# Performance work log

Hardware: AMD Instinct MI355X
Metric: run time of the kernel (lower is better)

## Reference

```python
import jax, jax.numpy as jnp
import numpy as np

WIN = 64
DF = 512
NH = 8
DH = DF // NH


def setup_inputs() -> dict:
    key = jax.random.key(0)
    k1, k2, k3, k4, k5 = jax.random.split(key, 5)
    b, n_p = 8, 4096
    x = jax.random.normal(k1, (b, n_p, DF), dtype=jnp.float32)
    z = jax.random.normal(k2, (b, n_p, DF), dtype=jnp.float32)
    # torch nn.Linear weights: [out_features, in_features]
    w_qkv = jax.random.normal(k3, (3 * DF, DF), dtype=jnp.float32) * (DF ** -0.5)
    proj_w = jax.random.normal(k4, (DF, DF), dtype=jnp.float32) * (DF ** -0.5)
    proj_b = jax.random.normal(k5, (DF,), dtype=jnp.float32) * 0.01
    return {"x": x, "z": z, "w_qkv": w_qkv, "proj_w": proj_w, "proj_b": proj_b}


def reference(x, z, w_qkv, proj_w, proj_b):
    b, n_p, _ = x.shape
    n_w, w_s = n_p // WIN, WIN
    scale = DH ** -0.5
    # QKV projection (no bias): [b, n_p, 3*DF]
    qkv = jnp.einsum('bnd,ed->bne', x, w_qkv)
    qkv = qkv.reshape(b, n_w, w_s, 3, NH, DH)
    q = qkv[:, :, :, 0]  # [b, n_w, w_s, NH, DH]
    k = qkv[:, :, :, 1]
    v = qkv[:, :, :, 2]
    # per-window attention scores: [b, n_w, NH, w_s, w_s]
    attn = scale * jnp.einsum('bwqhd,bwkhd->bwhqk', q, k)
    attn = jax.nn.softmax(attn, axis=-1)
    out = jnp.einsum('bwhqk,bwkhd->bwqhd', attn, v)  # [b, n_w, w_s, NH, DH]
    out = out.reshape(b, n_p, DF)
    out = jnp.einsum('bnd,ed->bne', out, proj_w) + proj_b
    return out
```

## Files before the change

### kernel.cpp

```cpp
#include <hip/hip_runtime.h>
#include <hip/hip_bf16.h>
#include <stdint.h>

#define NP 4096
#define DF 512
#define NQ3 1536

using bf16x8 = __attribute__((ext_vector_type(8))) short;
using f32x4  = __attribute__((ext_vector_type(4))) float;

static __device__ __forceinline__ f32x4 mfma16(bf16x8 a, bf16x8 b, f32x4 c) {
    return __builtin_amdgcn_mfma_f32_16x16x32_bf16(a, b, c, 0, 0, 0);
}
static __device__ __forceinline__ f32x4 zero4() { f32x4 z = {0.f,0.f,0.f,0.f}; return z; }

static __device__ __forceinline__ int SWZ64(int row, int col) {
    return (row * 64 + col) ^ ((row & 7) << 3);
}

static __device__ __forceinline__ unsigned short f2bf(float f) {
    __hip_bfloat16 h = __float2bfloat16(f);
    return reinterpret_cast<unsigned short&>(h);
}

#define GLOAD_LDS16(gp, lp) __builtin_amdgcn_global_load_lds( \
    (const __attribute__((address_space(1))) uint32_t*)(gp), \
    (__attribute__((address_space(3))) uint32_t*)(lp), 16, 0, 0)

__global__ void convert_all(const float* __restrict__ x,
                            const float* __restrict__ wqkv,
                            const float* __restrict__ projw,
                            unsigned short* __restrict__ xb,
                            unsigned short* __restrict__ wqb,
                            unsigned short* __restrict__ pwb) {
    const int XQ = (8 * NP * DF) / 4;
    const int WQ = (3 * DF * DF) / 4;
    const int PQ = (DF * DF) / 4;
    int i = blockIdx.x * blockDim.x + threadIdx.x;
    const float* src; unsigned short* dst; int j;
    if (i < XQ)                { src = x;     dst = xb;  j = i; }
    else if (i < XQ + WQ)      { src = wqkv;  dst = wqb; j = i - XQ; }
    else if (i < XQ + WQ + PQ) { src = projw; dst = pwb; j = i - XQ - WQ; }
    else return;
    float4 v = *(const float4*)(src + (size_t)j * 4);
    ushort4 o;
    o.x = f2bf(v.x); o.y = f2bf(v.y); o.z = f2bf(v.z); o.w = f2bf(v.w);
    *(ushort4*)(dst + (size_t)j * 4) = o;
}

__launch_bounds__(256, 2)
__global__ void qkv_gemm(const __hip_bfloat16* __restrict__ A,
                         const __hip_bfloat16* __restrict__ Bt,
                         unsigned short* __restrict__ C) {
    __shared__ __hip_bfloat16 As[128 * 64];
    __shared__ __hip_bfloat16 Bs[128 * 64];

    const int tid  = threadIdx.x;
    const int wid  = tid >> 6;
    const int lane = tid & 63;
    const int ln16 = lane & 15;
    const int lg   = lane >> 4;
    const int wr   = wid >> 1;
    const int wc   = wid & 1;

    int wk = (blockIdx.x & 7) * 384 + (blockIdx.x >> 3);
    const int m0 = (wk / 12) * 128;
    const int n0 = (wk % 12) * 128;

    f32x4 acc[4][4];
    #pragma unroll
    for (int i = 0; i < 4; ++i)
        #pragma unroll
        for (int j = 0; j < 4; ++j) acc[i][j] = zero4();

    for (int kt = 0; kt < 8; ++kt) {
        int k0 = kt * 64;
        #pragma unroll
        for (int it = 0; it < 4; ++it) {
            int slot = it * 256 + tid;
            int row  = slot >> 3;
            int c    = slot & 7;
            int gc   = (c ^ (row & 7)) * 8;
            GLOAD_LDS16(A  + (size_t)(m0 + row) * DF + k0 + gc, &As[slot * 8]);
            GLOAD_LDS16(Bt + (size_t)(n0 + row) * DF + k0 + gc, &Bs[slot * 8]);
        }
        __syncthreads();
        #pragma unroll
        for (int kk = 0; kk < 2; ++kk) {
            int c0 = kk * 4 + lg;
            bf16x8 af[4], bfr[4];
            #pragma unroll
            for (int rt = 0; rt < 4; ++rt) {
                int r = wr * 64 + rt * 16 + ln16;
                af[rt] = *(const bf16x8*)&As[(r << 6) + ((c0 ^ (r & 7)) << 3)];
            }
            #pragma unroll
            for (int ct = 0; ct < 4; ++ct) {
                int r = wc * 64 + ct * 16 + ln16;
                bfr[ct] = *(const bf16x8*)&Bs[(r << 6) + ((c0 ^ (r & 7)) << 3)];
            }
            #pragma unroll
            for (int rt = 0; rt < 4; ++rt)
                #pragma unroll
                for (int ct = 0; ct < 4; ++ct)
                    acc[rt][ct] = mfma16(af[rt], bfr[ct], acc[rt][ct]);
        }
        __syncthreads();
    }

    #pragma unroll
    for (int rt = 0; rt < 4; ++rt)
        #pragma unroll
        for (int ct = 0; ct < 4; ++ct)
            #pragma unroll
            for (int j = 0; j < 4; ++j)
                C[(size_t)(m0 + wr * 64 + rt * 16 + lg * 4 + j) * NQ3
                  + n0 + wc * 64 + ct * 16 + ln16] = f2bf(acc[rt][ct][j]);
}

__launch_bounds__(256, 2)
__global__ void attn(const __hip_bfloat16* __restrict__ qkv,
                     unsigned short* __restrict__ aout) {
    __shared__ unsigned short lds[4][2][64 * 64];

    const int tid  = threadIdx.x;
    const int wid  = tid >> 6;
    const int lane = tid & 63;
    const int ln16 = lane & 15;
    const int lg   = lane >> 4;

    const int blk = blockIdx.x;
    const int bw  = blk >> 1;
    const int hh  = (blk & 1) * 4 + wid;
    const size_t tokbase = (size_t)bw * 64;
    const __hip_bfloat16* base = qkv + tokbase * NQ3;

    #pragma unroll
    for (int rt = 0; rt < 4; ++rt)
        #pragma unroll
        for (int ks = 0; ks < 2; ++ks) {
            bf16x8 vf = *(const bf16x8*)(base + (size_t)(rt * 16 + ln16) * NQ3
                                         + 2 * DF + hh * 64 + ks * 32 + lg * 8);
            #pragma unroll
            for (int i = 0; i < 8; ++i) {
                int d = ks * 32 + lg * 8 + i;
                lds[wid][1][SWZ64(d, rt * 16 + ln16)] = (unsigned short)vf[i];
            }
        }

    bf16x8 kf[4][2];
    #pragma unroll
    for (int ct = 0; ct < 4; ++ct)
        #pragma unroll
        for (int ks = 0; ks < 2; ++ks)
            kf[ct][ks] = *(const bf16x8*)(base + (size_t)(ct * 16 + ln16) * NQ3
                                          + DF + hh * 64 + ks * 32 + lg * 8);

    const float scale = 0.125f;
    #pragma unroll
    for (int rt = 0; rt < 4; ++rt) {
        bf16x8 qf[2];
        #pragma unroll
        for (int ks = 0; ks < 2; ++ks)
            qf[ks] = *(const bf16x8*)(base + (size_t)(rt * 16 + ln16) * NQ3
                                      + hh * 64 + ks * 32 + lg * 8);
        f32x4 s[4];
        #pragma unroll
        for (int ct = 0; ct < 4; ++ct) s[ct] = zero4();
        #pragma unroll
        for (int ks = 0; ks < 2; ++ks)
            #pragma unroll
            for (int ct = 0; ct < 4; ++ct)
                s[ct] = mfma16(qf[ks], kf[ct][ks], s[ct]);
        #pragma unroll
        for (int j = 0; j < 4; ++j) {
            float sv[4];
            float m = -1e30f;
            #pragma unroll
            for (int ct = 0; ct < 4; ++ct) { sv[ct] = s[ct][j] * scale; m = fmaxf(m, sv[ct]); }
            #pragma unroll
            for (int off = 1; off < 16; off <<= 1) m = fmaxf(m, __shfl_xor(m, off));
            float pv[4], sum = 0.f;
            #pragma unroll
            for (int ct = 0; ct < 4; ++ct) { pv[ct] = __expf(sv[ct] - m); sum += pv[ct]; }
            #pragma unroll
            for (int off = 1; off < 16; off <<= 1) sum += __shfl_xor(sum, off);
            float inv = 1.f / sum;
            int q = rt * 16 + lg * 4 + j;
            #pragma unroll
            for (int ct = 0; ct < 4; ++ct)
                lds[wid][0][SWZ64(q, ct * 16 + ln16)] = f2bf(pv[ct] * inv);
        }
    }

    bf16x8 vtf[4][2];
    #pragma unroll
    for (int ct = 0; ct < 4; ++ct)
        #pragma unroll
        for (int ks = 0; ks < 2; ++ks)
            vtf[ct][ks] = *(const bf16x8*)&lds[wid][1][SWZ64(ct * 16 + ln16,
                                                             ks * 32 + lg * 8)];
    #pragma unroll
    for (int rt = 0; rt < 4; ++rt) {
        bf16x8 pf[2];
        #pragma unroll
        for (int ks = 0; ks < 2; ++ks)
            pf[ks] = *(const bf16x8*)&lds[wid][0][SWZ64(rt * 16 + ln16,
                                                        ks * 32 + lg * 8)];
        f32x4 o[4];
        #pragma unroll
        for (int ct = 0; ct < 4; ++ct) o[ct] = zero4();
        #pragma unroll
        for (int ks = 0; ks < 2; ++ks)
            #pragma unroll
            for (int ct = 0; ct < 4; ++ct)
                o[ct] = mfma16(pf[ks], vtf[ct][ks], o[ct]);
        #pragma unroll
        for (int ct = 0; ct < 4; ++ct)
            #pragma unroll
            for (int j = 0; j < 4; ++j)
                aout[(tokbase + rt * 16 + lg * 4 + j) * DF + hh * 64
                     + ct * 16 + ln16] = f2bf(o[ct][j]);
    }
}

__launch_bounds__(256, 4)
__global__ void proj_gemm(const __hip_bfloat16* __restrict__ A,
                          const __hip_bfloat16* __restrict__ Bt,
                          const float* __restrict__ bias,
                          float* __restrict__ out) {
    __shared__ __hip_bfloat16 As[128 * 64];
    __shared__ __hip_bfloat16 Bs[128 * 64];

    const int tid  = threadIdx.x;
    const int wid  = tid >> 6;
    const int lane = tid & 63;
    const int ln16 = lane & 15;
    const int lg   = lane >> 4;
    const int wr   = wid >> 1;
    const int wc   = wid & 1;

    int wk = (blockIdx.x & 7) * 128 + (blockIdx.x >> 3);
    const int m0  = (wk >> 2) * 128;
    const int n0g = (wk & 3) * 128;

    f32x4 acc[4][4];
    #pragma unroll
    for (int i = 0; i < 4; ++i)
        #pragma unroll
        for (int j = 0; j < 4; ++j) acc[i][j] = zero4();

    for (int kt = 0; kt < 8; ++kt) {
        int k0 = kt * 64;
        #pragma unroll
        for (int it = 0; it < 4; ++it) {
            int slot = it * 256 + tid;
            int row  = slot >> 3;
            int c    = slot & 7;
            int gc   = (c ^ (row & 7)) * 8;
            GLOAD_LDS16(A  + (size_t)(m0  + row) * DF + k0 + gc, &As[slot * 8]);
            GLOAD_LDS16(Bt + (size_t)(n0g + row) * DF + k0 + gc, &Bs[slot * 8]);
        }
        __syncthreads();
        #pragma unroll
        for (int kk = 0; kk < 2; ++kk) {
            int c0 = kk * 4 + lg;
            bf16x8 af[4], bfr[4];
            #pragma unroll
            for (int rt = 0; rt < 4; ++rt) {
                int r = wr * 64 + rt * 16 + ln16;
                af[rt] = *(const bf16x8*)&As[(r << 6) + ((c0 ^ (r & 7)) << 3)];
            }
            #pragma unroll
            for (int ct = 0; ct < 4; ++ct) {
                int r = wc * 64 + ct * 16 + ln16;
                bfr[ct] = *(const bf16x8*)&Bs[(r << 6) + ((c0 ^ (r & 7)) << 3)];
            }
            #pragma unroll
            for (int rt = 0; rt < 4; ++rt)
                #pragma unroll
                for (int ct = 0; ct < 4; ++ct)
                    acc[rt][ct] = mfma16(af[rt], bfr[ct], acc[rt][ct]);
        }
        __syncthreads();
    }

    #pragma unroll
    for (int ct = 0; ct < 4; ++ct) {
        int col = n0g + wc * 64 + ct * 16 + ln16;
        float bv = bias[col];
        #pragma unroll
        for (int rt = 0; rt < 4; ++rt)
            #pragma unroll
            for (int j = 0; j < 4; ++j)
                out[(size_t)(m0 + wr * 64 + rt * 16 + lg * 4 + j) * DF + col] =
                    acc[rt][ct][j] + bv;
    }
}

extern "C" void kernel_launch(void* const* d_in, const int* in_sizes, int n_in,
                              void* d_out, int out_size, void* d_ws, size_t ws_size,
                              hipStream_t stream) {
    const float* x      = (const float*)d_in[0];
    const float* w_qkv  = (const float*)d_in[2];
    const float* proj_w = (const float*)d_in[3];
    const float* proj_b = (const float*)d_in[4];
    float* outp = (float*)d_out;

    const size_t NTOK = (size_t)8 * NP;
    unsigned short* xb   = (unsigned short*)d_ws;
    unsigned short* qkvb = xb + NTOK * DF;
    unsigned short* wqb  = qkvb + NTOK * NQ3;
    unsigned short* pwb  = wqb + 3 * DF * DF;
    unsigned short* aout = xb;

    convert_all<<<8704, 512, 0, stream>>>(x, w_qkv, proj_w, xb, wqb, pwb);

    qkv_gemm<<<3072, 256, 0, stream>>>((const __hip_bfloat16*)xb,
                                       (const __hip_bfloat16*)wqb, qkvb);

    attn<<<1024, 256, 0, stream>>>((const __hip_bfloat16*)qkvb, aout);

    proj_gemm<<<1024, 256, 0, stream>>>((const __hip_bfloat16*)aout,
                                        (const __hip_bfloat16*)pwb,
                                        proj_b, outp);
}
```

Baseline: 131.1 us.

## Fuse x conversion into QKV GEMM and projection into attention kernel

Drops the separate fp32-to-bf16 pass over x: the QKV GEMM now loads fp32 x directly, converts it in registers and writes swizzled bf16 into LDS. The attention kernel now handles all 8 heads of a window per 512-thread block, stages each head's output in LDS, and runs the output projection plus bias in-block, so the standalone projection GEMM and its intermediate global round trip go away. In exchange, x is reread as fp32 once per column tile of the QKV GEMM instead of as bf16, that A tile no longer uses the async global-to-LDS path, and the projection reads weights straight from global memory without LDS reuse.

```diff
diff --git a/kernel.cpp b/kernel.cpp
--- a/kernel.cpp
+++ b/kernel.cpp
@@ -7,6 +7,7 @@
 #define NQ3 1536
 
 using bf16x8 = __attribute__((ext_vector_type(8))) short;
+using u16x8  = __attribute__((ext_vector_type(8))) unsigned short;
 using f32x4  = __attribute__((ext_vector_type(4))) float;
 
 static __device__ __forceinline__ f32x4 mfma16(bf16x8 a, bf16x8 b, f32x4 c) {
@@ -27,20 +28,16 @@
     (const __attribute__((address_space(1))) uint32_t*)(gp), \
     (__attribute__((address_space(3))) uint32_t*)(lp), 16, 0, 0)
 
-__global__ void convert_all(const float* __restrict__ x,
-                            const float* __restrict__ wqkv,
-                            const float* __restrict__ projw,
-                            unsigned short* __restrict__ xb,
-                            unsigned short* __restrict__ wqb,
-                            unsigned short* __restrict__ pwb) {
-    const int XQ = (8 * NP * DF) / 4;
+__global__ void convert_weights(const float* __restrict__ wqkv,
+                                const float* __restrict__ projw,
+                                unsigned short* __restrict__ wqb,
+                                unsigned short* __restrict__ pwb) {
     const int WQ = (3 * DF * DF) / 4;
     const int PQ = (DF * DF) / 4;
     int i = blockIdx.x * blockDim.x + threadIdx.x;
     const float* src; unsigned short* dst; int j;
-    if (i < XQ)                { src = x;     dst = xb;  j = i; }
-    else if (i < XQ + WQ)      { src = wqkv;  dst = wqb; j = i - XQ; }
-    else if (i < XQ + WQ + PQ) { src = projw; dst = pwb; j = i - XQ - WQ; }
+    if (i < WQ)           { src = wqkv;  dst = wqb; j = i; }
+    else if (i < WQ + PQ) { src = projw; dst = pwb; j = i - WQ; }
     else return;
     float4 v = *(const float4*)(src + (size_t)j * 4);
     ushort4 o;
@@ -49,7 +46,7 @@
 }
 
 __launch_bounds__(256, 2)
-__global__ void qkv_gemm(const __hip_bfloat16* __restrict__ A,
+__global__ void qkv_gemm(const float* __restrict__ A,
                          const __hip_bfloat16* __restrict__ Bt,
                          unsigned short* __restrict__ C) {
     __shared__ __hip_bfloat16 As[128 * 64];
@@ -81,8 +78,20 @@
             int row  = slot >> 3;
             int c    = slot & 7;
             int gc   = (c ^ (row & 7)) * 8;
-            GLOAD_LDS16(A  + (size_t)(m0 + row) * DF + k0 + gc, &As[slot * 8]);
             GLOAD_LDS16(Bt + (size_t)(n0 + row) * DF + k0 + gc, &Bs[slot * 8]);
+        }
+        #pragma unroll
+        for (int it = 0; it < 4; ++it) {
+            int slot = it * 256 + tid;
+            int row  = slot >> 3;
+            int c    = slot & 7;
+            const float* gp = A + (size_t)(m0 + row) * DF + k0 + c * 8;
+            float4 v0 = *(const float4*)gp;
+            float4 v1 = *(const float4*)(gp + 4);
+            u16x8 u;
+            u[0] = f2bf(v0.x); u[1] = f2bf(v0.y); u[2] = f2bf(v0.z); u[3] = f2bf(v0.w);
+            u[4] = f2bf(v1.x); u[5] = f2bf(v1.y); u[6] = f2bf(v1.z); u[7] = f2bf(v1.w);
+            *(u16x8*)&As[row * 64 + (c ^ (row & 7)) * 8] = u;
         }
         __syncthreads();
         #pragma unroll
@@ -118,10 +127,12 @@
                   + n0 + wc * 64 + ct * 16 + ln16] = f2bf(acc[rt][ct][j]);
 }
 
-__launch_bounds__(256, 2)
-__global__ void attn(const __hip_bfloat16* __restrict__ qkv,
-                     unsigned short* __restrict__ aout) {
-    __shared__ unsigned short lds[4][2][64 * 64];
+__launch_bounds__(512, 2)
+__global__ void attn_proj(const __hip_bfloat16* __restrict__ qkv,
+                          const __hip_bfloat16* __restrict__ pw,
+                          const float* __restrict__ bias,
+                          float* __restrict__ out) {
+    __shared__ unsigned short lds[8][2][64 * 64];
 
     const int tid  = threadIdx.x;
     const int wid  = tid >> 6;
@@ -129,11 +140,10 @@
     const int ln16 = lane & 15;
     const int lg   = lane >> 4;
 
-    const int blk = blockIdx.x;
-    const int bw  = blk >> 1;
-    const int hh  = (blk & 1) * 4 + wid;
+    const int bw = blockIdx.x;
     const size_t tokbase = (size_t)bw * 64;
     const __hip_bfloat16* base = qkv + tokbase * NQ3;
+    const int hh = wid;
 
     #pragma unroll
     for (int rt = 0; rt < 4; ++rt)
@@ -144,7 +154,7 @@
             #pragma unroll
             for (int i = 0; i < 8; ++i) {
                 int d = ks * 32 + lg * 8 + i;
-                lds[wid][1][SWZ64(d, rt * 16 + ln16)] = (unsigned short)vf[i];
+                lds[hh][1][SWZ64(d, rt * 16 + ln16)] = (unsigned short)vf[i];
             }
         }
 
@@ -189,7 +199,7 @@
             int q = rt * 16 + lg * 4 + j;
             #pragma unroll
             for (int ct = 0; ct < 4; ++ct)
-                lds[wid][0][SWZ64(q, ct * 16 + ln16)] = f2bf(pv[ct] * inv);
+                lds[hh][0][SWZ64(q, ct * 16 + ln16)] = f2bf(pv[ct] * inv);
         }
     }
 
@@ -198,15 +208,15 @@
     for (int ct = 0; ct < 4; ++ct)
         #pragma unroll
         for (int ks = 0; ks < 2; ++ks)
-            vtf[ct][ks] = *(const bf16x8*)&lds[wid][1][SWZ64(ct * 16 + ln16,
-                                                             ks * 32 + lg * 8)];
+            vtf[ct][ks] = *(const bf16x8*)&lds[hh][1][SWZ64(ct * 16 + ln16,
+                                                            ks * 32 + lg * 8)];
     #pragma unroll
     for (int rt = 0; rt < 4; ++rt) {
         bf16x8 pf[2];
         #pragma unroll
         for (int ks = 0; ks < 2; ++ks)
-            pf[ks] = *(const bf16x8*)&lds[wid][0][SWZ64(rt * 16 + ln16,
-                                                        ks * 32 + lg * 8)];
+            pf[ks] = *(const bf16x8*)&lds[hh][0][SWZ64(rt * 16 + ln16,
+                                                       ks * 32 + lg * 8)];
         f32x4 o[4];
         #pragma unroll
         for (int ct = 0; ct < 4; ++ct) o[ct] = zero4();
@@ -219,82 +229,48 @@
         for (int ct = 0; ct < 4; ++ct)
             #pragma unroll
             for (int j = 0; j < 4; ++j)
-                aout[(tokbase + rt * 16 + lg * 4 + j) * DF + hh * 64
-                     + ct * 16 + ln16] = f2bf(o[ct][j]);
-    }
-}
-
-__launch_bounds__(256, 4)
-__global__ void proj_gemm(const __hip_bfloat16* __restrict__ A,
-                          const __hip_bfloat16* __restrict__ Bt,
-                          const float* __restrict__ bias,
-                          float* __restrict__ out) {
-    __shared__ __hip_bfloat16 As[128 * 64];
-    __shared__ __hip_bfloat16 Bs[128 * 64];
-
-    const int tid  = threadIdx.x;
-    const int wid  = tid >> 6;
-    const int lane = tid & 63;
-    const int ln16 = lane & 15;
-    const int lg   = lane >> 4;
-    const int wr   = wid >> 1;
-    const int wc   = wid & 1;
-
-    int wk = (blockIdx.x & 7) * 128 + (blockIdx.x >> 3);
-    const int m0  = (wk >> 2) * 128;
-    const int n0g = (wk & 3) * 128;
-
-    f32x4 acc[4][4];
+                lds[hh][1][SWZ64(rt * 16 + lg * 4 + j, ct * 16 + ln16)] =
+                    f2bf(o[ct][j]);
+    }
+    __syncthreads();
+
+    f32x4 oacc[4][4];
     #pragma unroll
     for (int i = 0; i < 4; ++i)
         #pragma unroll
-        for (int j = 0; j < 4; ++j) acc[i][j] = zero4();
-
-    for (int kt = 0; kt < 8; ++kt) {
-        int k0 = kt * 64;
-        #pragma unroll
-        for (int it = 0; it < 4; ++it) {
-            int slot = it * 256 + tid;
-            int row  = slot >> 3;
-            int c    = slot & 7;
-            int gc   = (c ^ (row & 7)) * 8;
-            GLOAD_LDS16(A  + (size_t)(m0  + row) * DF + k0 + gc, &As[slot * 8]);
-            GLOAD_LDS16(Bt + (size_t)(n0g + row) * DF + k0 + gc, &Bs[slot * 8]);
-        }
-        __syncthreads();
+        for (int j = 0; j < 4; ++j) oacc[i][j] = zero4();
+
+    for (int h2 = 0; h2 < 8; ++h2) {
         #pragma unroll
         for (int kk = 0; kk < 2; ++kk) {
-            int c0 = kk * 4 + lg;
-            bf16x8 af[4], bfr[4];
-            #pragma unroll
-            for (int rt = 0; rt < 4; ++rt) {
-                int r = wr * 64 + rt * 16 + ln16;
-                af[rt] = *(const bf16x8*)&As[(r << 6) + ((c0 ^ (r & 7)) << 3)];
-            }
+            int kl = kk * 32 + lg * 8;
+            bf16x8 a[4];
+            #pragma unroll
+            for (int rt = 0; rt < 4; ++rt)
+                a[rt] = *(const bf16x8*)&lds[h2][1][SWZ64(rt * 16 + ln16, kl)];
             #pragma unroll
             for (int ct = 0; ct < 4; ++ct) {
-                int r = wc * 64 + ct * 16 + ln16;
-                bfr[ct] = *(const bf16x8*)&Bs[(r << 6) + ((c0 ^ (r & 7)) << 3)];
-            }
-            #pragma unroll
-            for (int rt = 0; rt < 4; ++rt)
+                const __hip_bfloat16* prow =
+                    (const __hip_bfloat16*)pw
+                    + ((size_t)(wid * 64 + ct * 16 + ln16)) * DF + h2 * 64 + kl;
+                bf16x8 bfr = *(const bf16x8*)prow;
                 #pragma unroll
-                for (int ct = 0; ct < 4; ++ct)
-                    acc[rt][ct] = mfma16(af[rt], bfr[ct], acc[rt][ct]);
-        }
-        __syncthreads();
+                for (int rt = 0; rt < 4; ++rt)
+                    oacc[rt][ct] = mfma16(a[rt], bfr, oacc[rt][ct]);
+            }
+        }
     }
 
     #pragma unroll
     for (int ct = 0; ct < 4; ++ct) {
-        int col = n0g + wc * 64 + ct * 16 + ln16;
+        int col = wid * 64 + ct * 16 + ln16;
         float bv = bias[col];
         #pragma unroll
         for (int rt = 0; rt < 4; ++rt)
             #pragma unroll
             for (int j = 0; j < 4; ++j)
-                out[(size_t)(m0 + wr * 64 + rt * 16 + lg * 4 + j) * DF + col] =
-                    acc[rt][ct][j] + bv;
+                out[(tokbase + rt * 16 + lg * 4 + j) * DF + col] =
+                    oacc[rt][ct][j] + bv;
     }
 }
 
@@ -308,20 +284,15 @@
     float* outp = (float*)d_out;
 
     const size_t NTOK = (size_t)8 * NP;
-    unsigned short* xb   = (unsigned short*)d_ws;
-    unsigned short* qkvb = xb + NTOK * DF;
+    unsigned short* qkvb = (unsigned short*)d_ws;
     unsigned short* wqb  = qkvb + NTOK * NQ3;
     unsigned short* pwb  = wqb + 3 * DF * DF;
-    unsigned short* aout = xb;
-
-    convert_all<<<8704, 512, 0, stream>>>(x, w_qkv, proj_w, xb, wqb, pwb);
-
-    qkv_gemm<<<3072, 256, 0, stream>>>((const __hip_bfloat16*)xb,
-                                       (const __hip_bfloat16*)wqb, qkvb);
-
-    attn<<<1024, 256, 0, stream>>>((const __hip_bfloat16*)qkvb, aout);
-
-    proj_gemm<<<1024, 256, 0, stream>>>((const __hip_bfloat16*)aout,
-                                        (const __hip_bfloat16*)pwb,
-                                        proj_b, outp);
-}
+
+    convert_weights<<<512, 512, 0, stream>>>(w_qkv, proj_w, wqb, pwb);
+
+    qkv_gemm<<<3072, 256, 0, stream>>>(x, (const __hip_bfloat16*)wqb, qkvb);
+
+    attn_proj<<<512, 512, 0, stream>>>((const __hip_bfloat16*)qkvb,
+                                       (const __hip_bfloat16*)pwb,
+                                       proj_b, outp);
+}
```

Result: slower. 148.1 us (+13.0%).

## Enlarge QKV GEMM tile to 256x256 with double-buffered LDS prefetch

Applied to the files above, without the earlier changes.

The QKV projection GEMM moves from 128x128 tiles with 4 waves to 256x256 tiles with 8 waves, each wave computing a 128x64 sub-tile. Global-to-LDS loads are now double-buffered two k-steps ahead, using explicit vmcnt waits and barriers, so loads overlap with MFMA work. This is meant to raise arithmetic intensity per tile and hide memory latency. In exchange it uses 128KB of LDS per block and more accumulator registers, which limits occupancy, and the grid shrinks to 768 blocks.

```diff
diff --git a/kernel.cpp b/kernel.cpp
--- a/kernel.cpp
+++ b/kernel.cpp
@@ -48,74 +48,106 @@
     *(ushort4*)(dst + (size_t)j * 4) = o;
 }
 
-__launch_bounds__(256, 2)
+__launch_bounds__(512, 2)
 __global__ void qkv_gemm(const __hip_bfloat16* __restrict__ A,
                          const __hip_bfloat16* __restrict__ Bt,
                          unsigned short* __restrict__ C) {
-    __shared__ __hip_bfloat16 As[128 * 64];
-    __shared__ __hip_bfloat16 Bs[128 * 64];
+    __shared__ __hip_bfloat16 As[2][256 * 64];
+    __shared__ __hip_bfloat16 Bs[2][256 * 64];
 
     const int tid  = threadIdx.x;
     const int wid  = tid >> 6;
     const int lane = tid & 63;
     const int ln16 = lane & 15;
     const int lg   = lane >> 4;
-    const int wr   = wid >> 1;
-    const int wc   = wid & 1;
-
-    int wk = (blockIdx.x & 7) * 384 + (blockIdx.x >> 3);
-    const int m0 = (wk / 12) * 128;
-    const int n0 = (wk % 12) * 128;
-
-    f32x4 acc[4][4];
-    #pragma unroll
-    for (int i = 0; i < 4; ++i)
-        #pragma unroll
-        for (int j = 0; j < 4; ++j) acc[i][j] = zero4();
-
-    for (int kt = 0; kt < 8; ++kt) {
+    const int wr   = wid >> 2;
+    const int wc   = wid & 3;
+
+    int wk = (blockIdx.x & 7) * 96 + (blockIdx.x >> 3);
+    const int m0 = (wk / 6) * 256;
+    const int n0 = (wk % 6) * 256;
+
+    f32x4 acc[8][4];
+    #pragma unroll
+    for (int m = 0; m < 8; ++m)
+        #pragma unroll
+        for (int n = 0; n < 4; ++n) acc[m][n] = zero4();
+
+    auto STAGE = [&](int buf, int kt) {
         int k0 = kt * 64;
         #pragma unroll
         for (int it = 0; it < 4; ++it) {
-            int slot = it * 256 + tid;
+            int slot = it * 512 + tid;
             int row  = slot >> 3;
             int c    = slot & 7;
             int gc   = (c ^ (row & 7)) * 8;
-            GLOAD_LDS16(A  + (size_t)(m0 + row) * DF + k0 + gc, &As[slot * 8]);
-            GLOAD_LDS16(Bt + (size_t)(n0 + row) * DF + k0 + gc, &Bs[slot * 8]);
-        }
-        __syncthreads();
+            GLOAD_LDS16(A + (size_t)(m0 + row) * DF + k0 + gc, &As[buf][slot * 8]);
+        }
+        #pragma unroll
+        for (int it = 0; it < 4; ++it) {
+            int slot = it * 512 + tid;
+            int row  = slot >> 3;
+            int c    = slot & 7;
+            int gc   = (c ^ (row & 7)) * 8;
+            GLOAD_LDS16(Bt + (size_t)(n0 + row) * DF + k0 + gc, &Bs[buf][slot * 8]);
+        }
+    };
+
+    auto COMPUTE = [&](int buf) {
         #pragma unroll
         for (int kk = 0; kk < 2; ++kk) {
             int c0 = kk * 4 + lg;
-            bf16x8 af[4], bfr[4];
-            #pragma unroll
-            for (int rt = 0; rt < 4; ++rt) {
-                int r = wr * 64 + rt * 16 + ln16;
-                af[rt] = *(const bf16x8*)&As[(r << 6) + ((c0 ^ (r & 7)) << 3)];
-            }
-            #pragma unroll
-            for (int ct = 0; ct < 4; ++ct) {
-                int r = wc * 64 + ct * 16 + ln16;
-                bfr[ct] = *(const bf16x8*)&Bs[(r << 6) + ((c0 ^ (r & 7)) << 3)];
-            }
-            #pragma unroll
-            for (int rt = 0; rt < 4; ++rt)
+            bf16x8 af[8], bfr[4];
+            #pragma unroll
+            for (int m = 0; m < 8; ++m) {
+                int r = wr * 128 + m * 16 + ln16;
+                af[m] = *(const bf16x8*)&As[buf][(r << 6) + ((c0 ^ (r & 7)) << 3)];
+            }
+            #pragma unroll
+            for (int n = 0; n < 4; ++n) {
+                int r = wc * 64 + n * 16 + ln16;
+                bfr[n] = *(const bf16x8*)&Bs[buf][(r << 6) + ((c0 ^ (r & 7)) << 3)];
+            }
+            #pragma unroll
+            for (int m = 0; m < 8; ++m)
                 #pragma unroll
-                for (int ct = 0; ct < 4; ++ct)
-                    acc[rt][ct] = mfma16(af[rt], bfr[ct], acc[rt][ct]);
-        }
-        __syncthreads();
-    }
-
-    #pragma unroll
-    for (int rt = 0; rt < 4; ++rt)
-        #pragma unroll
-        for (int ct = 0; ct < 4; ++ct)
+                for (int n = 0; n < 4; ++n)
+                    acc[m][n] = mfma16(af[m], bfr[n], acc[m][n]);
+        }
+    };
+
+    STAGE(0, 0);
+    STAGE(1, 1);
+    asm volatile("s_waitcnt vmcnt(8)" ::: "memory");
+    __builtin_amdgcn_sched_barrier(0);
+    __builtin_amdgcn_s_barrier();
+    __builtin_amdgcn_sched_barrier(0);
+
+    int cur = 0;
+    for (int t = 0; t < 8; ++t) {
+        COMPUTE(cur);
+        __builtin_amdgcn_sched_barrier(0);
+        __builtin_amdgcn_s_barrier();
+        __builtin_amdgcn_sched_barrier(0);
+        if (t + 2 < 8) STAGE(cur, t + 2);
+        if (t + 1 < 8) {
+            if (t + 2 < 8) { asm volatile("s_waitcnt vmcnt(8)" ::: "memory"); }
+            else           { asm volatile("s_waitcnt vmcnt(0)" ::: "memory"); }
+            __builtin_amdgcn_sched_barrier(0);
+            __builtin_amdgcn_s_barrier();
+            __builtin_amdgcn_sched_barrier(0);
+        }
+        cur ^= 1;
+    }
+
+    #pragma unroll
+    for (int m = 0; m < 8; ++m)
+        #pragma unroll
+        for (int n = 0; n < 4; ++n)
             #pragma unroll
             for (int j = 0; j < 4; ++j)
-                C[(size_t)(m0 + wr * 64 + rt * 16 + lg * 4 + j) * NQ3
-                  + n0 + wc * 64 + ct * 16 + ln16] = f2bf(acc[rt][ct][j]);
+                C[(size_t)(m0 + wr * 128 + m * 16 + lg * 4 + j) * NQ3
+                  + n0 + wc * 64 + n * 16 + ln16] = f2bf(acc[m][n][j]);
 }
 
 __launch_bounds__(256, 2)
@@ -316,8 +348,8 @@
 
     convert_all<<<8704, 512, 0, stream>>>(x, w_qkv, proj_w, xb, wqb, pwb);
 
-    qkv_gemm<<<3072, 256, 0, stream>>>((const __hip_bfloat16*)xb,
-                                       (const __hip_bfloat16*)wqb, qkvb);
+    qkv_gemm<<<768, 512, 0, stream>>>((const __hip_bfloat16*)xb,
+                                      (const __hip_bfloat16*)wqb, qkvb);
 
     attn<<<1024, 256, 0, stream>>>((const __hip_bfloat16*)qkvb, aout);
 
```

Result: slower. 142.5 us (+8.7%).

## Fuse fp32-to-bf16 conversion of x into QKV GEMM tile loads

Applied to the files above, without the earlier changes.

Removes the separate pass that converted the full activation tensor x to bf16 in workspace. The QKV GEMM now streams fp32 x tiles into LDS with an XOR swizzle and converts them to bf16 while building the MFMA fragments. Only the weights are still pre-converted by a small kernel. This saves a full read and write of x in a separate launch, at the cost of double LDS footprint and bandwidth for A, extra conversion ALU in the inner loop, and fp32 re-reads of x across the N-tiles.

```diff
diff --git a/kernel.cpp b/kernel.cpp
--- a/kernel.cpp
+++ b/kernel.cpp
@@ -27,20 +27,16 @@
     (const __attribute__((address_space(1))) uint32_t*)(gp), \
     (__attribute__((address_space(3))) uint32_t*)(lp), 16, 0, 0)
 
-__global__ void convert_all(const float* __restrict__ x,
-                            const float* __restrict__ wqkv,
-                            const float* __restrict__ projw,
-                            unsigned short* __restrict__ xb,
-                            unsigned short* __restrict__ wqb,
-                            unsigned short* __restrict__ pwb) {
-    const int XQ = (8 * NP * DF) / 4;
+__global__ void convert_weights(const float* __restrict__ wqkv,
+                                const float* __restrict__ projw,
+                                unsigned short* __restrict__ wqb,
+                                unsigned short* __restrict__ pwb) {
     const int WQ = (3 * DF * DF) / 4;
     const int PQ = (DF * DF) / 4;
     int i = blockIdx.x * blockDim.x + threadIdx.x;
     const float* src; unsigned short* dst; int j;
-    if (i < XQ)                { src = x;     dst = xb;  j = i; }
-    else if (i < XQ + WQ)      { src = wqkv;  dst = wqb; j = i - XQ; }
-    else if (i < XQ + WQ + PQ) { src = projw; dst = pwb; j = i - XQ - WQ; }
+    if (i < WQ)           { src = wqkv;  dst = wqb; j = i; }
+    else if (i < WQ + PQ) { src = projw; dst = pwb; j = i - WQ; }
     else return;
     float4 v = *(const float4*)(src + (size_t)j * 4);
     ushort4 o;
@@ -49,11 +45,11 @@
 }
 
 __launch_bounds__(256, 2)
-__global__ void qkv_gemm(const __hip_bfloat16* __restrict__ A,
+__global__ void qkv_gemm(const float* __restrict__ A,
                          const __hip_bfloat16* __restrict__ Bt,
                          unsigned short* __restrict__ C) {
-    __shared__ __hip_bfloat16 As[128 * 64];
-    __shared__ __hip_bfloat16 Bs[128 * 64];
+    __shared__ float           Asf[128 * 64];
+    __shared__ __hip_bfloat16  Bs [128 * 64];
 
     const int tid  = threadIdx.x;
     const int wid  = tid >> 6;
@@ -76,28 +72,45 @@
     for (int kt = 0; kt < 8; ++kt) {
         int k0 = kt * 64;
         #pragma unroll
+        for (int it = 0; it < 8; ++it) {
+            int slot = it * 256 + tid;
+            int row  = slot >> 4;
+            int c    = slot & 15;
+            int gc   = c ^ ((row & 7) << 1);
+            GLOAD_LDS16(A + (size_t)(m0 + row) * DF + k0 + gc * 4, &Asf[slot * 4]);
+        }
+        #pragma unroll
         for (int it = 0; it < 4; ++it) {
             int slot = it * 256 + tid;
             int row  = slot >> 3;
             int c    = slot & 7;
             int gc   = (c ^ (row & 7)) * 8;
-            GLOAD_LDS16(A  + (size_t)(m0 + row) * DF + k0 + gc, &As[slot * 8]);
             GLOAD_LDS16(Bt + (size_t)(n0 + row) * DF + k0 + gc, &Bs[slot * 8]);
         }
         __syncthreads();
         #pragma unroll
         for (int kk = 0; kk < 2; ++kk) {
-            int c0 = kk * 4 + lg;
             bf16x8 af[4], bfr[4];
+            int c0 = kk * 8 + lg * 2;
             #pragma unroll
             for (int rt = 0; rt < 4; ++rt) {
-                int r = wr * 64 + rt * 16 + ln16;
-                af[rt] = *(const bf16x8*)&As[(r << 6) + ((c0 ^ (r & 7)) << 3)];
-            }
+                int r    = wr * 64 + rt * 16 + ln16;
+                int base = (r << 6) + ((c0 ^ ((r & 7) << 1)) << 2);
+                f32x4 lo = *(const f32x4*)&Asf[base];
+                f32x4 hi = *(const f32x4*)&Asf[base + 4];
+                bf16x8 a;
+                #pragma unroll
+                for (int i = 0; i < 4; ++i) {
+                    a[i]     = (short)f2bf(lo[i]);
+                    a[i + 4] = (short)f2bf(hi[i]);
+                }
+                af[rt] = a;
+            }
+            int c0b = kk * 4 + lg;
             #pragma unroll
             for (int ct = 0; ct < 4; ++ct) {
                 int r = wc * 64 + ct * 16 + ln16;
-                bfr[ct] = *(const bf16x8*)&Bs[(r << 6) + ((c0 ^ (r & 7)) << 3)];
+                bfr[ct] = *(const bf16x8*)&Bs[(r << 6) + ((c0b ^ (r & 7)) << 3)];
             }
             #pragma unroll
             for (int rt = 0; rt < 4; ++rt)
@@ -308,16 +321,14 @@
     float* outp = (float*)d_out;
 
     const size_t NTOK = (size_t)8 * NP;
-    unsigned short* xb   = (unsigned short*)d_ws;
-    unsigned short* qkvb = xb + NTOK * DF;
+    unsigned short* qkvb = (unsigned short*)d_ws;
     unsigned short* wqb  = qkvb + NTOK * NQ3;
     unsigned short* pwb  = wqb + 3 * DF * DF;
-    unsigned short* aout = xb;
-
-    convert_all<<<8704, 512, 0, stream>>>(x, w_qkv, proj_w, xb, wqb, pwb);
-
-    qkv_gemm<<<3072, 256, 0, stream>>>((const __hip_bfloat16*)xb,
-                                       (const __hip_bfloat16*)wqb, qkvb);
+    unsigned short* aout = pwb + DF * DF;
+
+    convert_weights<<<512, 512, 0, stream>>>(w_qkv, proj_w, wqb, pwb);
+
+    qkv_gemm<<<3072, 256, 0, stream>>>(x, (const __hip_bfloat16*)wqb, qkvb);
 
     attn<<<1024, 256, 0, stream>>>((const __hip_bfloat16*)qkvb, aout);
 
```

New measurement: 173.1 us. +32.0%, slower.
